# Performance work log

Hardware: AMD Instinct MI355X
Metric: run time of the kernel (lower is better)

The kernel has to match this reference:

```python
import jax, jax.numpy as jnp
import numpy as np

N_NODES = 50000


def gcn_conv(x, src, dst, W, b, n_nodes):
    """PyG GCNConv: out = D^-1/2 (A + I) D^-1/2 (x W) + b.
    Self-loop contribution added analytically (norm = dinv[i]^2)."""
    h = x @ W  # [N, out]
    ones = jnp.ones(dst.shape[0], dtype=x.dtype)
    deg = jax.ops.segment_sum(ones, dst, num_segments=n_nodes) + 1.0  # +1 self-loop
    dinv = jax.lax.rsqrt(deg)
    norm = dinv[src] * dinv[dst]  # [E]
    msg = h[src] * norm[:, None]  # [E, out] gathered messages
    agg = jax.ops.segment_sum(msg, dst, num_segments=n_nodes)
    agg = agg + h * (dinv * dinv)[:, None]  # self-loop term
    return agg + b


def encode(x, edge_index, W1, b1, W2, b2, n_nodes):
    src, dst = edge_index[0], edge_index[1]
    x = jax.nn.relu(gcn_conv(x, src, dst, W1, b1, n_nodes))
    x = jax.nn.relu(gcn_conv(x, src, dst, W2, b2, n_nodes))
    return x


def setup_inputs() -> dict:
    key = jax.random.key(0)
    ks = jax.random.split(key, 8)
    E = 800000
    in_c, hid2, hid = 128, 256, 128
    x_a = jax.random.normal(ks[0], (N_NODES, in_c), dtype=jnp.float32)
    x_b = jax.random.normal(ks[1], (N_NODES, in_c), dtype=jnp.float32)
    edge_a = jax.random.randint(ks[2], (2, E), 0, N_NODES, dtype=jnp.int64)
    edge_b = jax.random.randint(ks[3], (2, E), 0, N_NODES, dtype=jnp.int64)
    W1 = jax.random.normal(ks[4], (in_c, hid2), dtype=jnp.float32) * (1.0 / np.sqrt(in_c))
    b1 = jnp.zeros((hid2,), dtype=jnp.float32)
    W2 = jax.random.normal(ks[5], (hid2, hid), dtype=jnp.float32) * (1.0 / np.sqrt(hid2))
    b2 = jnp.zeros((hid,), dtype=jnp.float32)
    return {"x_a": x_a, "edge_a": edge_a, "x_b": x_b, "edge_b": edge_b,
            "W1": W1, "b1": b1, "W2": W2, "b2": b2}


def reference(x_a, edge_a, x_b, edge_b, W1, b1, W2, b2):
    z_a = encode(x_a, edge_a, W1, b1, W2, b2, N_NODES)
    z_b = encode(x_b, edge_b, W1, b1, W2, b2, N_NODES)
    return (z_a, z_b)
```

## Files before the change

### kernel.cpp

```cpp
#include <hip/hip_runtime.h>

#define NN 50000

typedef __attribute__((ext_vector_type(8))) short s16x8;
typedef __attribute__((ext_vector_type(8))) unsigned short u16x8;
typedef __attribute__((ext_vector_type(4))) float f32x4;

__device__ inline unsigned short f2bf(float f) {
    unsigned u = __float_as_uint(f);
    u += 0x7fff + ((u >> 16) & 1);
    return (unsigned short)(u >> 16);
}
__device__ inline float bf2f(unsigned short h) { return __uint_as_float((unsigned)h << 16); }

__global__ __launch_bounds__(256) void k_deg(const int* __restrict__ dst, int E,
                                             int* __restrict__ deg) {
    int e = blockIdx.x * 256 + threadIdx.x;
    if (e < E) atomicAdd(&deg[dst[e]], 1);
}

__global__ __launch_bounds__(1024) void k_bsum_dinv(const int* __restrict__ deg,
                                                    float* __restrict__ dinv,
                                                    int* __restrict__ bsum, int n) {
    const int tid = threadIdx.x;
    const int i = blockIdx.x * 1024 + tid;
    int v = 0;
    if (i < n) {
        v = deg[i];
        dinv[i] = rsqrtf((float)v + 1.0f);
    }
    int s = v;
#pragma unroll
    for (int off = 32; off; off >>= 1) s += __shfl_down(s, off, 64);
    __shared__ int ws[16];
    if ((tid & 63) == 0) ws[tid >> 6] = s;
    __syncthreads();
    if (tid < 16) {
        int t = ws[tid];
#pragma unroll
        for (int off = 8; off; off >>= 1) t += __shfl_down(t, off, 16);
        if (tid == 0) bsum[blockIdx.x] = t;
    }
}

__global__ __launch_bounds__(64) void k_pscan(const int* __restrict__ bsum,
                                              int* __restrict__ boff, int nb,
                                              int* __restrict__ rowp_last, int E) {
    const int tid = threadIdx.x;
    int v = (tid < nb) ? bsum[tid] : 0;
    int s = v;
#pragma unroll
    for (int off = 1; off < 64; off <<= 1) {
        int t = __shfl_up(s, off, 64);
        if (tid >= off) s += t;
    }
    if (tid < nb) boff[tid] = s - v;
    if (tid == 0) *rowp_last = E;
}

__global__ __launch_bounds__(1024) void k_scan2(const int* __restrict__ deg,
                                                const int* __restrict__ boff,
                                                int* __restrict__ rowp,
                                                int* __restrict__ cursor, int n) {
    const int tid = threadIdx.x;
    const int i = blockIdx.x * 1024 + tid;
    const int wid = tid >> 6, lane = tid & 63;
    int v = (i < n) ? deg[i] : 0;
    int s = v;
#pragma unroll
    for (int off = 1; off < 64; off <<= 1) {
        int t = __shfl_up(s, off, 64);
        if (lane >= off) s += t;
    }
    __shared__ int ws[16];
    if (lane == 63) ws[wid] = s;
    __syncthreads();
    if (wid == 0) {
        int t = (lane < 16) ? ws[lane] : 0;
#pragma unroll
        for (int off = 1; off < 16; off <<= 1) {
            int u = __shfl_up(t, off, 64);
            if (lane >= off) t += u;
        }
        if (lane < 16) ws[lane] = t;
    }
    __syncthreads();
    const int woff = wid ? ws[wid - 1] : 0;
    if (i < n) {
        int excl = boff[blockIdx.x] + woff + s - v;
        rowp[i] = excl;
        cursor[i] = excl;
    }
}

__global__ __launch_bounds__(256) void k_bin(const int* __restrict__ src,
                                             const int* __restrict__ dst,
                                             int* __restrict__ cursor,
                                             unsigned short* __restrict__ e_src, int E) {
    int e = blockIdx.x * 256 + threadIdx.x;
    if (e >= E) return;
    int slot = atomicAdd(&cursor[dst[e]], 1);
    e_src[slot] = (unsigned short)src[e];
}

__global__ __launch_bounds__(256) void k_cvt_bf(const float* __restrict__ in,
                                                unsigned short* __restrict__ out, int n4) {
    int i = blockIdx.x * 256 + threadIdx.x;
    if (i >= n4) return;
    float4 v = ((const float4*)in)[i];
    ((ushort4*)out)[i] = make_ushort4(f2bf(v.x), f2bf(v.y), f2bf(v.z), f2bf(v.w));
}

__global__ __launch_bounds__(256) void k_wcvt(const float* __restrict__ W,
                                              unsigned short* __restrict__ Wh,
                                              unsigned short* __restrict__ Wl,
                                              int K, int N) {
    int idx = blockIdx.x * 256 + threadIdx.x;
    if (idx >= K * N) return;
    int k = idx / N, n = idx % N;
    float v = W[idx];
    unsigned short h = f2bf(v);
    unsigned short l = f2bf(v - bf2f(h));
    int klo = k & 31;
    int pos = (k & ~31) + ((klo & 15) >> 2) * 8 + ((klo >> 4) & 1) * 4 + (klo & 3);
    Wh[(size_t)n * K + pos] = h;
    Wl[(size_t)n * K + pos] = l;
}

template <bool EPI, bool OUTBF>
__global__ __launch_bounds__(256) void mgemm(const float* __restrict__ A,
                                             const unsigned short* __restrict__ Wh,
                                             const unsigned short* __restrict__ Wl,
                                             const float* __restrict__ bias,
                                             void* __restrict__ Cv,
                                             int M, int N, int K) {
    __shared__ unsigned short Ah[64 * 64], Al[64 * 64];
    __shared__ unsigned short Bh[64 * 64], Bl[64 * 64];
    const int tid = threadIdx.x;
    const int bm = blockIdx.y * 64;
    const int bn = blockIdx.x * 64;
    const int wid = tid >> 6, lane = tid & 63;
    const int wr = (wid >> 1) * 32, wc = (wid & 1) * 32;
    const int l15 = lane & 15, lg = lane >> 4;

    f32x4 acc[2][2] = {};

    const int srow = tid >> 4;
    const int sk0 = (tid & 15) * 4;
    const int sb = (sk0 >> 5) * 64 + (((sk0 & 15) >> 2) * 8 + ((sk0 >> 4) & 1) * 4) * 2;
    const int bcol = tid >> 2;
    const int bck = (tid & 3) * 32;

    for (int kt = 0; kt < K; kt += 64) {
#pragma unroll
        for (int p = 0; p < 4; ++p) {
            const int row = p * 16 + srow;
            const int gr = bm + row;
            float4 v = make_float4(0.f, 0.f, 0.f, 0.f);
            if (gr < M) v = *(const float4*)&A[(size_t)gr * K + kt + sk0];
            const unsigned short h0 = f2bf(v.x), h1 = f2bf(v.y), h2 = f2bf(v.z), h3 = f2bf(v.w);
            const unsigned short l0 = f2bf(v.x - bf2f(h0)), l1 = f2bf(v.y - bf2f(h1));
            const unsigned short l2 = f2bf(v.z - bf2f(h2)), l3 = f2bf(v.w - bf2f(h3));
            const int byte = sb ^ ((row & 7) << 4);
            *(ushort4*)((char*)Ah + row * 128 + byte) = make_ushort4(h0, h1, h2, h3);
            *(ushort4*)((char*)Al + row * 128 + byte) = make_ushort4(l0, l1, l2, l3);
        }
        {
            const unsigned short* gh = &Wh[(size_t)(bn + bcol) * K + kt + (bck >> 1)];
            const unsigned short* gl = &Wl[(size_t)(bn + bcol) * K + kt + (bck >> 1)];
            const int byt0 = bck ^ ((bcol & 7) << 4);
            const int byt1 = (bck + 16) ^ ((bcol & 7) << 4);
            *(u16x8*)((char*)Bh + bcol * 128 + byt0) = *(const u16x8*)gh;
            *(u16x8*)((char*)Bh + bcol * 128 + byt1) = *(const u16x8*)(gh + 8);
            *(u16x8*)((char*)Bl + bcol * 128 + byt0) = *(const u16x8*)gl;
            *(u16x8*)((char*)Bl + bcol * 128 + byt1) = *(const u16x8*)(gl + 8);
        }
        __syncthreads();
#pragma unroll
        for (int kk = 0; kk < 2; ++kk) {
            s16x8 ah[2], al[2], bh[2], bl[2];
#pragma unroll
            for (int rf = 0; rf < 2; ++rf) {
                const int row = wr + rf * 16 + l15;
                const int byte = (kk * 64 + lg * 16) ^ ((row & 7) << 4);
                ah[rf] = *(const s16x8*)((const char*)Ah + row * 128 + byte);
                al[rf] = *(const s16x8*)((const char*)Al + row * 128 + byte);
            }
#pragma unroll
            for (int cf = 0; cf < 2; ++cf) {
                const int col = wc + cf * 16 + l15;
                const int byte = (kk * 64 + lg * 16) ^ ((col & 7) << 4);
                bh[cf] = *(const s16x8*)((const char*)Bh + col * 128 + byte);
                bl[cf] = *(const s16x8*)((const char*)Bl + col * 128 + byte);
            }
#pragma unroll
            for (int rf = 0; rf < 2; ++rf)
#pragma unroll
                for (int cf = 0; cf < 2; ++cf) {
                    acc[rf][cf] = __builtin_amdgcn_mfma_f32_16x16x32_bf16(ah[rf], bh[cf],
                                                                          acc[rf][cf], 0, 0, 0);
                    acc[rf][cf] = __builtin_amdgcn_mfma_f32_16x16x32_bf16(ah[rf], bl[cf],
                                                                          acc[rf][cf], 0, 0, 0);
                    acc[rf][cf] = __builtin_amdgcn_mfma_f32_16x16x32_bf16(al[rf], bh[cf],
                                                                          acc[rf][cf], 0, 0, 0);
                }
        }
        __syncthreads();
    }
#pragma unroll
    for (int rf = 0; rf < 2; ++rf)
#pragma unroll
        for (int cf = 0; cf < 2; ++cf) {
            const int col = bn + wc + cf * 16 + l15;
            const float bv = EPI ? bias[col] : 0.f;
#pragma unroll
            for (int r = 0; r < 4; ++r) {
                const int gr = bm + wr + rf * 16 + lg * 4 + r;
                if (gr < M) {
                    float v = acc[rf][cf][r];
                    if (EPI) v = fmaxf(v + bv, 0.f);
                    if constexpr (OUTBF)
                        ((unsigned short*)Cv)[(size_t)gr * N + col] = f2bf(v);
                    else
                        ((float*)Cv)[(size_t)gr * N + col] = v;
                }
            }
        }
}

template <bool BIAS_RELU>
__global__ __launch_bounds__(256) void k_agg(const int* __restrict__ row_ptr,
                                             const unsigned short* __restrict__ e_src,
                                             const unsigned short* __restrict__ hb,
                                             const float* __restrict__ dinv,
                                             const float* __restrict__ bias,
                                             float* __restrict__ out, int n) {
    constexpr int C = 128;
    const int node = (blockIdx.x * 256 + threadIdx.x) >> 6;
    const int lane = threadIdx.x & 63;
    if (node >= n) return;
    const int beg = row_ptr[node], end = row_ptr[node + 1];
    const float dn = dinv[node];

    float a0 = 0.f, a1 = 0.f;
    int e = beg;
    for (; e + 3 < end; e += 4) {
        const int s0 = e_src[e + 0], s1 = e_src[e + 1];
        const int s2 = e_src[e + 2], s3 = e_src[e + 3];
        const float n0 = dinv[s0] * dn, n1 = dinv[s1] * dn;
        const float n2 = dinv[s2] * dn, n3 = dinv[s3] * dn;
        const unsigned v0 = *(const unsigned*)&hb[(size_t)s0 * C + lane * 2];
        const unsigned v1 = *(const unsigned*)&hb[(size_t)s1 * C + lane * 2];
        const unsigned v2 = *(const unsigned*)&hb[(size_t)s2 * C + lane * 2];
        const unsigned v3 = *(const unsigned*)&hb[(size_t)s3 * C + lane * 2];
        a0 += __uint_as_float(v0 << 16) * n0 + __uint_as_float(v1 << 16) * n1 +
              __uint_as_float(v2 << 16) * n2 + __uint_as_float(v3 << 16) * n3;
        a1 += __uint_as_float(v0 & 0xffff0000u) * n0 + __uint_as_float(v1 & 0xffff0000u) * n1 +
              __uint_as_float(v2 & 0xffff0000u) * n2 + __uint_as_float(v3 & 0xffff0000u) * n3;
    }
    for (; e < end; ++e) {
        const int s = e_src[e];
        const float nr = dinv[s] * dn;
        const unsigned v = *(const unsigned*)&hb[(size_t)s * C + lane * 2];
        a0 += __uint_as_float(v << 16) * nr;
        a1 += __uint_as_float(v & 0xffff0000u) * nr;
    }
    const unsigned vs = *(const unsigned*)&hb[(size_t)node * C + lane * 2];
    const float d2 = dn * dn;
    a0 += __uint_as_float(vs << 16) * d2;
    a1 += __uint_as_float(vs & 0xffff0000u) * d2;
    if constexpr (BIAS_RELU) {
        const float2 bv = *(const float2*)&bias[lane * 2];
        a0 = fmaxf(a0 + bv.x, 0.f);
        a1 = fmaxf(a1 + bv.y, 0.f);
    }
    *(float2*)&out[(size_t)node * C + lane * 2] = make_float2(a0, a1);
}

extern "C" void kernel_launch(void* const* d_in, const int* in_sizes, int n_in,
                              void* d_out, int out_size, void* d_ws, size_t ws_size,
                              hipStream_t stream) {
    const float* x[2] = {(const float*)d_in[0], (const float*)d_in[2]};
    const int* eidx[2] = {(const int*)d_in[1], (const int*)d_in[3]};
    const int E[2] = {in_sizes[1] / 2, in_sizes[3] / 2};
    const float* W1 = (const float*)d_in[4];
    const float* b1 = (const float*)d_in[5];
    const float* W2 = (const float*)d_in[6];
    const float* b2 = (const float*)d_in[7];
    float* out = (float*)d_out;

    const int Emax = (E[0] > E[1]) ? E[0] : E[1];
    char* ws = (char*)d_ws;
    size_t off = 0;
    auto alloc = [&](size_t bytes) -> void* {
        void* p = ws + off;
        off = (off + bytes + 255) & ~(size_t)255;
        return p;
    };
    float* aggX = (float*)alloc((size_t)NN * 128 * 4);
    float* x1 = (float*)alloc((size_t)NN * 256 * 4);
    unsigned short* x_bf = (unsigned short*)alloc((size_t)NN * 128 * 2);
    unsigned short* h2_bf = (unsigned short*)alloc((size_t)NN * 128 * 2);
    unsigned short* W1h = (unsigned short*)alloc(128 * 256 * 2);
    unsigned short* W1l = (unsigned short*)alloc(128 * 256 * 2);
    unsigned short* W2h = (unsigned short*)alloc(256 * 128 * 2);
    unsigned short* W2l = (unsigned short*)alloc(256 * 128 * 2);
    int* deg = (int*)alloc((size_t)NN * 4);
    float* dinv = (float*)alloc((size_t)NN * 4);
    int* rowp = (int*)alloc((size_t)(NN + 1) * 4);
    int* cursor = (int*)alloc((size_t)NN * 4);
    int* bsum = (int*)alloc(64 * 4);
    int* boff = (int*)alloc(64 * 4);
    unsigned short* e_src = (unsigned short*)alloc((size_t)Emax * 2);

    const int NB = (NN + 1023) / 1024;

    k_wcvt<<<(128 * 256 + 255) / 256, 256, 0, stream>>>(W1, W1h, W1l, 128, 256);
    k_wcvt<<<(256 * 128 + 255) / 256, 256, 0, stream>>>(W2, W2h, W2l, 256, 128);

    for (int g = 0; g < 2; ++g) {
        const int Eg = E[g];
        const int* srcp = eidx[g];
        const int* dstp = eidx[g] + Eg;

        hipMemsetAsync(deg, 0, NN * sizeof(int), stream);
        k_cvt_bf<<<(NN * 128 / 4 + 255) / 256, 256, 0, stream>>>(x[g], x_bf, NN * 128 / 4);
        k_deg<<<(Eg + 255) / 256, 256, 0, stream>>>(dstp, Eg, deg);
        k_bsum_dinv<<<NB, 1024, 0, stream>>>(deg, dinv, bsum, NN);
        k_pscan<<<1, 64, 0, stream>>>(bsum, boff, NB, &rowp[NN], Eg);
        k_scan2<<<NB, 1024, 0, stream>>>(deg, boff, rowp, cursor, NN);
        k_bin<<<(Eg + 255) / 256, 256, 0, stream>>>(srcp, dstp, cursor, e_src, Eg);

        k_agg<false><<<(NN + 3) / 4, 256, 0, stream>>>(rowp, e_src, x_bf, dinv, nullptr,
                                                       aggX, NN);
        mgemm<true, false><<<dim3(256 / 64, (NN + 63) / 64), 256, 0, stream>>>(
            aggX, W1h, W1l, b1, x1, NN, 256, 128);

        mgemm<false, true><<<dim3(128 / 64, (NN + 63) / 64), 256, 0, stream>>>(
            x1, W2h, W2l, nullptr, h2_bf, NN, 128, 256);
        k_agg<true><<<(NN + 3) / 4, 256, 0, stream>>>(rowp, e_src, h2_bf, dinv, b2,
                                                      out + (size_t)g * NN * 128, NN);
    }
}
```

Baseline: 579.7 us.

## Store layer-1 activations in bf16 and split aggregation edges across half-waves

The first GEMM now writes its ReLU output as bf16 instead of fp32. The second GEMM reads those bf16 activations directly, which removes the hi/lo split of A and one of its three MFMA passes. Separately, the aggregation kernel has each half-wave process alternate edges with 8-byte loads per lane, then combines the two halves with a cross-lane shuffle. This halves the intermediate activation traffic and cuts GEMM compute, at the cost of lower precision for the layer-1 activations.

```diff
diff --git a/kernel.cpp b/kernel.cpp
--- a/kernel.cpp
+++ b/kernel.cpp
@@ -12,6 +12,8 @@
     return (unsigned short)(u >> 16);
 }
 __device__ inline float bf2f(unsigned short h) { return __uint_as_float((unsigned)h << 16); }
+__device__ inline float blo(unsigned u) { return __uint_as_float(u << 16); }
+__device__ inline float bhi(unsigned u) { return __uint_as_float(u & 0xffff0000u); }
 
 __global__ __launch_bounds__(256) void k_deg(const int* __restrict__ dst, int E,
                                              int* __restrict__ deg) {
@@ -127,14 +129,15 @@
     Wl[(size_t)n * K + pos] = l;
 }
 
-template <bool EPI, bool OUTBF>
-__global__ __launch_bounds__(256) void mgemm(const float* __restrict__ A,
+template <bool EPI, bool OUTBF, bool ABF>
+__global__ __launch_bounds__(256) void mgemm(const void* __restrict__ Av,
                                              const unsigned short* __restrict__ Wh,
                                              const unsigned short* __restrict__ Wl,
                                              const float* __restrict__ bias,
                                              void* __restrict__ Cv,
                                              int M, int N, int K) {
-    __shared__ unsigned short Ah[64 * 64], Al[64 * 64];
+    __shared__ unsigned short Ah[64 * 64];
+    __shared__ unsigned short Al[(ABF ? 1 : 64) * 64];
     __shared__ unsigned short Bh[64 * 64], Bl[64 * 64];
     const int tid = threadIdx.x;
     const int bm = blockIdx.y * 64;
@@ -143,27 +146,51 @@
     const int wr = (wid >> 1) * 32, wc = (wid & 1) * 32;
     const int l15 = lane & 15, lg = lane >> 4;
 
+    const float* Af = (const float*)Av;
+    const unsigned short* Ab = (const unsigned short*)Av;
+
     f32x4 acc[2][2] = {};
 
     const int srow = tid >> 4;
     const int sk0 = (tid & 15) * 4;
     const int sb = (sk0 >> 5) * 64 + (((sk0 & 15) >> 2) * 8 + ((sk0 >> 4) & 1) * 4) * 2;
+    const int srow2 = tid >> 3;
+    const int sk0b = (tid & 7) * 8;
+    const int sb0 = (sk0b >> 5) * 64 + (((sk0b & 15) >> 2) * 8 + ((sk0b >> 4) & 1) * 4) * 2;
+    const int sk1b = sk0b + 4;
+    const int sb1 = (sk1b >> 5) * 64 + (((sk1b & 15) >> 2) * 8 + ((sk1b >> 4) & 1) * 4) * 2;
     const int bcol = tid >> 2;
     const int bck = (tid & 3) * 32;
 
     for (int kt = 0; kt < K; kt += 64) {
-#pragma unroll
-        for (int p = 0; p < 4; ++p) {
-            const int row = p * 16 + srow;
-            const int gr = bm + row;
-            float4 v = make_float4(0.f, 0.f, 0.f, 0.f);
-            if (gr < M) v = *(const float4*)&A[(size_t)gr * K + kt + sk0];
-            const unsigned short h0 = f2bf(v.x), h1 = f2bf(v.y), h2 = f2bf(v.z), h3 = f2bf(v.w);
-            const unsigned short l0 = f2bf(v.x - bf2f(h0)), l1 = f2bf(v.y - bf2f(h1));
-            const unsigned short l2 = f2bf(v.z - bf2f(h2)), l3 = f2bf(v.w - bf2f(h3));
-            const int byte = sb ^ ((row & 7) << 4);
-            *(ushort4*)((char*)Ah + row * 128 + byte) = make_ushort4(h0, h1, h2, h3);
-            *(ushort4*)((char*)Al + row * 128 + byte) = make_ushort4(l0, l1, l2, l3);
+        if constexpr (!ABF) {
+#pragma unroll
+            for (int p = 0; p < 4; ++p) {
+                const int row = p * 16 + srow;
+                const int gr = bm + row;
+                float4 v = make_float4(0.f, 0.f, 0.f, 0.f);
+                if (gr < M) v = *(const float4*)&Af[(size_t)gr * K + kt + sk0];
+                const unsigned short h0 = f2bf(v.x), h1 = f2bf(v.y), h2 = f2bf(v.z),
+                                     h3 = f2bf(v.w);
+                const unsigned short l0 = f2bf(v.x - bf2f(h0)), l1 = f2bf(v.y - bf2f(h1));
+                const unsigned short l2 = f2bf(v.z - bf2f(h2)), l3 = f2bf(v.w - bf2f(h3));
+                const int byte = sb ^ ((row & 7) << 4);
+                *(ushort4*)((char*)Ah + row * 128 + byte) = make_ushort4(h0, h1, h2, h3);
+                *(ushort4*)((char*)Al + row * 128 + byte) = make_ushort4(l0, l1, l2, l3);
+            }
+        } else {
+#pragma unroll
+            for (int p = 0; p < 2; ++p) {
+                const int row = p * 32 + srow2;
+                const int gr = bm + row;
+                u16x8 v = {0, 0, 0, 0, 0, 0, 0, 0};
+                if (gr < M) v = *(const u16x8*)&Ab[(size_t)gr * K + kt + sk0b];
+                const int sw = (row & 7) << 4;
+                *(ushort4*)((char*)Ah + row * 128 + (sb0 ^ sw)) =
+                    make_ushort4(v[0], v[1], v[2], v[3]);
+                *(ushort4*)((char*)Ah + row * 128 + (sb1 ^ sw)) =
+                    make_ushort4(v[4], v[5], v[6], v[7]);
+            }
         }
         {
             const unsigned short* gh = &Wh[(size_t)(bn + bcol) * K + kt + (bck >> 1)];
@@ -184,7 +211,8 @@
                 const int row = wr + rf * 16 + l15;
                 const int byte = (kk * 64 + lg * 16) ^ ((row & 7) << 4);
                 ah[rf] = *(const s16x8*)((const char*)Ah + row * 128 + byte);
-                al[rf] = *(const s16x8*)((const char*)Al + row * 128 + byte);
+                if constexpr (!ABF)
+                    al[rf] = *(const s16x8*)((const char*)Al + row * 128 + byte);
             }
 #pragma unroll
             for (int cf = 0; cf < 2; ++cf) {
@@ -201,8 +229,9 @@
                                                                           acc[rf][cf], 0, 0, 0);
                     acc[rf][cf] = __builtin_amdgcn_mfma_f32_16x16x32_bf16(ah[rf], bl[cf],
                                                                           acc[rf][cf], 0, 0, 0);
-                    acc[rf][cf] = __builtin_amdgcn_mfma_f32_16x16x32_bf16(al[rf], bh[cf],
-                                                                          acc[rf][cf], 0, 0, 0);
+                    if constexpr (!ABF)
+                        acc[rf][cf] = __builtin_amdgcn_mfma_f32_16x16x32_bf16(
+                            al[rf], bh[cf], acc[rf][cf], 0, 0, 0);
                 }
         }
         __syncthreads();
@@ -235,46 +264,68 @@
                                              const float* __restrict__ dinv,
                                              const float* __restrict__ bias,
                                              float* __restrict__ out, int n) {
-    constexpr int C = 128;
     const int node = (blockIdx.x * 256 + threadIdx.x) >> 6;
     const int lane = threadIdx.x & 63;
+    const int half = lane >> 5, l32 = lane & 31;
     if (node >= n) return;
     const int beg = row_ptr[node], end = row_ptr[node + 1];
     const float dn = dinv[node];
 
-    float a0 = 0.f, a1 = 0.f;
+    float a0 = 0.f, a1 = 0.f, a2 = 0.f, a3 = 0.f;
     int e = beg;
-    for (; e + 3 < end; e += 4) {
-        const int s0 = e_src[e + 0], s1 = e_src[e + 1];
-        const int s2 = e_src[e + 2], s3 = e_src[e + 3];
+    for (; e + 7 < end; e += 8) {
+        const int s0 = e_src[e + half], s1 = e_src[e + 2 + half];
+        const int s2 = e_src[e + 4 + half], s3 = e_src[e + 6 + half];
         const float n0 = dinv[s0] * dn, n1 = dinv[s1] * dn;
         const float n2 = dinv[s2] * dn, n3 = dinv[s3] * dn;
-        const unsigned v0 = *(const unsigned*)&hb[(size_t)s0 * C + lane * 2];
-        const unsigned v1 = *(const unsigned*)&hb[(size_t)s1 * C + lane * 2];
-        const unsigned v2 = *(const unsigned*)&hb[(size_t)s2 * C + lane * 2];
-        const unsigned v3 = *(const unsigned*)&hb[(size_t)s3 * C + lane * 2];
-        a0 += __uint_as_float(v0 << 16) * n0 + __uint_as_float(v1 << 16) * n1 +
-              __uint_as_float(v2 << 16) * n2 + __uint_as_float(v3 << 16) * n3;
-        a1 += __uint_as_float(v0 & 0xffff0000u) * n0 + __uint_as_float(v1 & 0xffff0000u) * n1 +
-              __uint_as_float(v2 & 0xffff0000u) * n2 + __uint_as_float(v3 & 0xffff0000u) * n3;
-    }
-    for (; e < end; ++e) {
+        const uint2 v0 = *(const uint2*)&hb[(size_t)s0 * 128 + l32 * 4];
+        const uint2 v1 = *(const uint2*)&hb[(size_t)s1 * 128 + l32 * 4];
+        const uint2 v2 = *(const uint2*)&hb[(size_t)s2 * 128 + l32 * 4];
+        const uint2 v3 = *(const uint2*)&hb[(size_t)s3 * 128 + l32 * 4];
+        a0 += blo(v0.x) * n0 + blo(v1.x) * n1 + blo(v2.x) * n2 + blo(v3.x) * n3;
+        a1 += bhi(v0.x) * n0 + bhi(v1.x) * n1 + bhi(v2.x) * n2 + bhi(v3.x) * n3;
+        a2 += blo(v0.y) * n0 + blo(v1.y) * n1 + blo(v2.y) * n2 + blo(v3.y) * n3;
+        a3 += bhi(v0.y) * n0 + bhi(v1.y) * n1 + bhi(v2.y) * n2 + bhi(v3.y) * n3;
+    }
+    for (; e + 1 < end; e += 2) {
+        const int s = e_src[e + half];
+        const float nr = dinv[s] * dn;
+        const uint2 v = *(const uint2*)&hb[(size_t)s * 128 + l32 * 4];
+        a0 += blo(v.x) * nr;
+        a1 += bhi(v.x) * nr;
+        a2 += blo(v.y) * nr;
+        a3 += bhi(v.y) * nr;
+    }
+    if (e < end && half == 0) {
         const int s = e_src[e];
         const float nr = dinv[s] * dn;
-        const unsigned v = *(const unsigned*)&hb[(size_t)s * C + lane * 2];
-        a0 += __uint_as_float(v << 16) * nr;
-        a1 += __uint_as_float(v & 0xffff0000u) * nr;
-    }
-    const unsigned vs = *(const unsigned*)&hb[(size_t)node * C + lane * 2];
-    const float d2 = dn * dn;
-    a0 += __uint_as_float(vs << 16) * d2;
-    a1 += __uint_as_float(vs & 0xffff0000u) * d2;
-    if constexpr (BIAS_RELU) {
-        const float2 bv = *(const float2*)&bias[lane * 2];
-        a0 = fmaxf(a0 + bv.x, 0.f);
-        a1 = fmaxf(a1 + bv.y, 0.f);
-    }
-    *(float2*)&out[(size_t)node * C + lane * 2] = make_float2(a0, a1);
+        const uint2 v = *(const uint2*)&hb[(size_t)s * 128 + l32 * 4];
+        a0 += blo(v.x) * nr;
+        a1 += bhi(v.x) * nr;
+        a2 += blo(v.y) * nr;
+        a3 += bhi(v.y) * nr;
+    }
+    a0 += __shfl_xor(a0, 32, 64);
+    a1 += __shfl_xor(a1, 32, 64);
+    a2 += __shfl_xor(a2, 32, 64);
+    a3 += __shfl_xor(a3, 32, 64);
+
+    if (half == 0) {
+        const uint2 vs = *(const uint2*)&hb[(size_t)node * 128 + l32 * 4];
+        const float d2 = dn * dn;
+        a0 += blo(vs.x) * d2;
+        a1 += bhi(vs.x) * d2;
+        a2 += blo(vs.y) * d2;
+        a3 += bhi(vs.y) * d2;
+        if constexpr (BIAS_RELU) {
+            const float4 bv = *(const float4*)&bias[l32 * 4];
+            a0 = fmaxf(a0 + bv.x, 0.f);
+            a1 = fmaxf(a1 + bv.y, 0.f);
+            a2 = fmaxf(a2 + bv.z, 0.f);
+            a3 = fmaxf(a3 + bv.w, 0.f);
+        }
+        *(float4*)&out[(size_t)node * 128 + l32 * 4] = make_float4(a0, a1, a2, a3);
+    }
 }
 
 extern "C" void kernel_launch(void* const* d_in, const int* in_sizes, int n_in,
@@ -298,7 +349,7 @@
         return p;
     };
     float* aggX = (float*)alloc((size_t)NN * 128 * 4);
-    float* x1 = (float*)alloc((size_t)NN * 256 * 4);
+    unsigned short* x1_bf = (unsigned short*)alloc((size_t)NN * 256 * 2);
     unsigned short* x_bf = (unsigned short*)alloc((size_t)NN * 128 * 2);
     unsigned short* h2_bf = (unsigned short*)alloc((size_t)NN * 128 * 2);
     unsigned short* W1h = (unsigned short*)alloc(128 * 256 * 2);
@@ -333,11 +384,11 @@
 
         k_agg<false><<<(NN + 3) / 4, 256, 0, stream>>>(rowp, e_src, x_bf, dinv, nullptr,
                                                        aggX, NN);
-        mgemm<true, false><<<dim3(256 / 64, (NN + 63) / 64), 256, 0, stream>>>(
-            aggX, W1h, W1l, b1, x1, NN, 256, 128);
-
-        mgemm<false, true><<<dim3(128 / 64, (NN + 63) / 64), 256, 0, stream>>>(
-            x1, W2h, W2l, nullptr, h2_bf, NN, 128, 256);
+        mgemm<true, true, false><<<dim3(256 / 64, (NN + 63) / 64), 256, 0, stream>>>(
+            aggX, W1h, W1l, b1, x1_bf, NN, 256, 128);
+
+        mgemm<false, true, true><<<dim3(128 / 64, (NN + 63) / 64), 256, 0, stream>>>(
+            x1_bf, W2h, W2l, nullptr, h2_bf, NN, 128, 256);
         k_agg<true><<<(NN + 3) / 4, 256, 0, stream>>>(rowp, e_src, h2_bf, dinv, b2,
                                                       out + (size_t)g * NN * 128, NN);
     }
```

Measured after the change: 534.9 us. -7.7%, faster.
